# Optimization experiments

Hardware: AMD Instinct MI355X
Metric: run time of the kernel (lower is better)

Reference implementation:

```python
import jax, jax.numpy as jnp
import numpy as np

# ---- module hyperparameters (from init_kwargs) ----
DIM = 16        # Hilbert-space dimension (density matrix is DIM x DIM)
BATCH = 32      # number of initial states evolved in parallel
K_LIND = 4      # number of Lindblad collapse operators
N_TS = 512      # number of Euler integration steps
N_CTRLS = 4     # number of control channels
N_PARAMS = 16   # B-spline control points per channel
DEGREE = 3      # cubic B-splines
T_TOTAL = 1.0
DT = T_TOTAL / N_TS


def _bspline_basis_matrix(t, knots, degree):
    """Cox-de Boor recursion, vectorized over all basis functions.
    t: (n_ts,), knots: (n_knots,). Returns (n_ts, n_knots-1-degree)."""
    k = knots
    # degree-0: indicator of half-open knot spans -> (n_ts, n_knots-1)
    B = ((k[None, :-1] <= t[:, None]) & (t[:, None] < k[None, 1:])).astype(t.dtype)
    for d in range(1, degree + 1):
        left_den = k[d:-1] - k[:-(d + 1)]
        right_den = k[d + 1:] - k[1:-d]
        left = jnp.where(left_den > 0,
                         (t[:, None] - k[None, :-(d + 1)]) / jnp.where(left_den > 0, left_den, 1.0) * B[:, :-1],
                         0.0)
        right = jnp.where(right_den > 0,
                          (k[None, d + 1:] - t[:, None]) / jnp.where(right_den > 0, right_den, 1.0) * B[:, 1:],
                          0.0)
        B = left + right
    return B  # (n_ts, n_knots - 1 - degree) == (n_ts, N_PARAMS)


def setup_inputs() -> dict:
    key = jax.random.key(0)
    ks = jax.random.split(key, 10)
    f32 = jnp.float32
    params = 0.5 * jax.random.normal(ks[0], (N_PARAMS, N_CTRLS), f32)
    H0_re = jax.random.normal(ks[1], (DIM, DIM), f32)
    H0_im = jax.random.normal(ks[2], (DIM, DIM), f32)
    Hc_re = jax.random.normal(ks[3], (N_CTRLS, DIM, DIM), f32)
    Hc_im = jax.random.normal(ks[4], (N_CTRLS, DIM, DIM), f32)
    L_re = 0.3 * jax.random.normal(ks[5], (K_LIND, DIM, DIM), f32)
    L_im = 0.3 * jax.random.normal(ks[6], (K_LIND, DIM, DIM), f32)
    # valid density matrices: rho0 = A A^dag / tr(A A^dag)
    A = (jax.random.normal(ks[7], (BATCH, DIM, DIM), f32)
         + 1j * jax.random.normal(ks[8], (BATCH, DIM, DIM), f32)).astype(jnp.complex64)
    rho0 = jnp.einsum('bij,bkj->bik', A, A.conj())
    tr = jnp.trace(rho0, axis1=-2, axis2=-1).real[:, None, None]
    rho0 = rho0 / tr.astype(jnp.complex64)
    return {
        'params': params,
        'H0_re': H0_re, 'H0_im': H0_im,
        'Hc_re': Hc_re, 'Hc_im': Hc_im,
        'L_re': L_re, 'L_im': L_im,
        'rho0_re': jnp.real(rho0).astype(f32),
        'rho0_im': jnp.imag(rho0).astype(f32),
    }


def reference(params, H0_re, H0_im, Hc_re, Hc_im, L_re, L_im, rho0_re, rho0_im):
    c64 = jnp.complex64
    # Hermitize Hamiltonians
    H0 = (H0_re + 1j * H0_im).astype(c64)
    H0 = 0.5 * (H0 + H0.conj().T)
    Hc = (Hc_re + 1j * Hc_im).astype(c64)
    Hc = 0.5 * (Hc + jnp.conj(jnp.swapaxes(Hc, -1, -2)))
    L = (L_re + 1j * L_im).astype(c64)              # (K, d, d)
    LdL = jnp.einsum('kji,kjl->il', L.conj(), L)    # sum_k L^dag L  (d, d)
    rho0 = (rho0_re + 1j * rho0_im).astype(c64)     # (B, d, d)

    # B-spline control pulses (clamped knot vector, as in evaluate_bspline_batch)
    t = jnp.arange(N_TS, dtype=jnp.float32) * DT
    knots = jnp.concatenate([
        jnp.zeros(DEGREE, jnp.float32),
        jnp.linspace(0.0, T_TOTAL, N_PARAMS - DEGREE + 1).astype(jnp.float32),
        T_TOTAL * jnp.ones(DEGREE, jnp.float32),
    ])
    basis = _bspline_basis_matrix(t, knots, DEGREE)  # (n_ts, n_params)
    u = basis @ params                               # (n_ts, n_ctrls)

    def step(rho, u_t):
        H = H0 + jnp.einsum('c,cij->ij', u_t.astype(c64), Hc)
        jump = jnp.einsum('kij,bjl,kml->bim', L, rho, L.conj())
        drho = (-1j) * (H @ rho - rho @ H) + jump - 0.5 * (LdL @ rho + rho @ LdL)
        rho_new = rho + DT * drho
        pops = jnp.real(jnp.diagonal(rho_new, axis1=-2, axis2=-1)).astype(jnp.float32)
        return rho_new, pops

    _, pops = jax.lax.scan(step, rho0, u)
    return pops  # (n_ts, batch, dim) real populations
```

## Files before the change

### kernel.cpp

```cpp
#include <hip/hip_runtime.h>
#include <hip/hip_bf16.h>

#define DIM    16
#define BATCH  32
#define KL     4
#define NTS    512
#define NC     4
#define NPAR   16
#define DTF    (1.0f/512.0f)
#define BST    40
#define FST    20
#define TST    36

using short8  = __attribute__((ext_vector_type(8))) short;
using short4v = __attribute__((ext_vector_type(4))) short;
using f32x4   = __attribute__((ext_vector_type(4))) float;

__device__ __forceinline__ float b2f(__hip_bfloat16 x) { return __bfloat162float(x); }

__device__ __forceinline__ float ldval(const void* p, int idx, bool isf32) {
  return isf32 ? ((const float*)p)[idx]
               : __bfloat162float(((const __hip_bfloat16*)p)[idx]);
}
__device__ __forceinline__ unsigned short f2bf(float x) {
  unsigned u = __float_as_uint(x);
  unsigned r = u + 0x7FFFu + ((u >> 16) & 1u);
  return (unsigned short)(r >> 16);
}
__device__ __forceinline__ float bf2f(unsigned short h) {
  return __uint_as_float(((unsigned)h) << 16);
}
__device__ __forceinline__ void split2(float v, unsigned short& h, unsigned short& l) {
  unsigned u = __float_as_uint(v);
  h = (unsigned short)(u >> 16);
  float r = v - __uint_as_float(u & 0xFFFF0000u);
  l = (unsigned short)(__float_as_uint(r) >> 16);
}
__device__ __forceinline__ unsigned splitpack(float v) {
  unsigned short h, l;
  split2(v, h, l);
  return (unsigned)h | ((unsigned)l << 16);
}
__device__ __forceinline__ short8 ldfrag(const unsigned short* p) {
  return *(const short8*)p;
}
__device__ __forceinline__ short8 negbf8(short8 a) {
  union { short8 s; unsigned u[4]; } v; v.s = a;
  #pragma unroll
  for (int q = 0; q < 4; ++q) v.u[q] ^= 0x80008000u;
  return v.s;
}
__device__ __forceinline__ f32x4 mm3(short8 Ah, short8 Al, short8 Bh, short8 Bl, f32x4 acc) {
  acc = __builtin_amdgcn_mfma_f32_16x16x32_bf16(Ah, Bh, acc, 0, 0, 0);
  acc = __builtin_amdgcn_mfma_f32_16x16x32_bf16(Al, Bh, acc, 0, 0, 0);
  acc = __builtin_amdgcn_mfma_f32_16x16x32_bf16(Ah, Bl, acc, 0, 0, 0);
  return acc;
}
__device__ __forceinline__ void packfrag(const float* v, short8& hi, short8& lo) {
  union { short8 s; unsigned short e[8]; } H, L;
  #pragma unroll
  for (int q = 0; q < 8; ++q) split2(v[q], H.e[q], L.e[q]);
  hi = H.s; lo = L.s;
}
__device__ __forceinline__ void ldfrag_paired(const unsigned* p, short8& hi, short8& lo) {
  uint4 wa = *(const uint4*)p;
  uint4 wb = *(const uint4*)(p + 4);
  union { short8 s; unsigned u[4]; } H, L;
  H.u[0] = __builtin_amdgcn_perm(wa.y, wa.x, 0x05040100u);
  H.u[1] = __builtin_amdgcn_perm(wa.w, wa.z, 0x05040100u);
  H.u[2] = __builtin_amdgcn_perm(wb.y, wb.x, 0x05040100u);
  H.u[3] = __builtin_amdgcn_perm(wb.w, wb.z, 0x05040100u);
  L.u[0] = __builtin_amdgcn_perm(wa.y, wa.x, 0x07060302u);
  L.u[1] = __builtin_amdgcn_perm(wa.w, wa.z, 0x07060302u);
  L.u[2] = __builtin_amdgcn_perm(wb.y, wb.x, 0x07060302u);
  L.u[3] = __builtin_amdgcn_perm(wb.w, wb.z, 0x07060302u);
  hi = H.s; lo = L.s;
}

__global__ __launch_bounds__(512, 1)
void lindblad_evolve(const void* __restrict__ g_params,
                     const void* __restrict__ g_H0re, const void* __restrict__ g_H0im,
                     const void* __restrict__ g_Hcre, const void* __restrict__ g_Hcim,
                     const void* __restrict__ g_Lre,  const void* __restrict__ g_Lim,
                     const void* __restrict__ g_r0re, const void* __restrict__ g_r0im,
                     float* __restrict__ g_out)
{
  __shared__ __align__(16) unsigned short sPh[16*BST], sPl[16*BST];
  __shared__ __align__(16) unsigned sTp[KL][16*TST];
  __shared__ __align__(16) unsigned short sLh[KL][16*BST], sLl[KL][16*BST];
  __shared__ __align__(16) float sMr[16*FST], sMi[16*FST];
  __shared__ __align__(16) float sU[NTS][NC];
  __shared__ __align__(16) float sPops[NTS*DIM];
  __shared__ int sFlag;

  const int tid = threadIdx.x;
  const int b   = blockIdx.x;
  const int i   = tid >> 4;
  const int j   = tid & 15;
  const int wv  = tid >> 6;
  const int ln  = tid & 63;
  const int fm  = ln & 15;
  const int fq  = ln >> 4;
  const int row0 = fq * 4;
  const int fOff  = fm*BST + fq*8;
  const int fOffS = fm*BST + ((fq*8 + 16) & 31);

  if (tid == 0) sFlag = 0;
  __syncthreads();
  if (tid < 256) {
    float v = b2f(((const __hip_bfloat16*)g_H0re)[tid]);
    if (!(fabsf(v) <= 1e10f)) atomicOr(&sFlag, 1);
  }
  __syncthreads();
  const bool isf32 = (sFlag != 0);

  {
    float kn[20];
    kn[0] = 0.f; kn[1] = 0.f; kn[2] = 0.f;
    #pragma unroll
    for (int q = 0; q < 14; ++q) kn[3 + q] = (float)q / 13.0f;
    kn[17] = 1.f; kn[18] = 1.f; kn[19] = 1.f;
    const float t = (float)tid * DTF;
    float B[19];
    #pragma unroll
    for (int q = 0; q < 19; ++q) B[q] = (kn[q] <= t && t < kn[q+1]) ? 1.f : 0.f;
    #pragma unroll
    for (int d = 1; d <= 3; ++d) {
      #pragma unroll
      for (int q = 0; q + d < 19; ++q) {
        float ld = kn[q+d]   - kn[q];
        float rd = kn[q+d+1] - kn[q+1];
        float lv = (ld > 0.f) ? (t - kn[q])     / ld * B[q]   : 0.f;
        float rv = (rd > 0.f) ? (kn[q+d+1] - t) / rd * B[q+1] : 0.f;
        B[q] = lv + rv;
      }
    }
    #pragma unroll
    for (int c = 0; c < NC; ++c) {
      float s = 0.f;
      #pragma unroll
      for (int q = 0; q < NPAR; ++q) s += B[q] * ldval(g_params, q*NC + c, isf32);
      sU[tid][c] = s;
    }
  }

  if (tid < 256) {
    float* scr = sPops;
    const int ij = i*16 + j, ji = j*16 + i;
    float h0r = 0.5f * (ldval(g_H0re, ij, isf32) + ldval(g_H0re, ji, isf32));
    float h0i = 0.5f * (ldval(g_H0im, ij, isf32) - ldval(g_H0im, ji, isf32));
    float ldr = 0.f, ldi = 0.f;
    for (int k = 0; k < KL; ++k) {
      #pragma unroll
      for (int m = 0; m < DIM; ++m) {
        float ar = ldval(g_Lre, k*256 + m*16 + i, isf32), ai = ldval(g_Lim, k*256 + m*16 + i, isf32);
        float br = ldval(g_Lre, k*256 + m*16 + j, isf32), bi = ldval(g_Lim, k*256 + m*16 + j, isf32);
        ldr += ar*br + ai*bi;
        ldi += ar*bi - ai*br;
      }
    }
    scr[0*256 + ij] =  h0i - 0.5f*ldr;
    scr[1*256 + ij] = -h0r - 0.5f*ldi;
    #pragma unroll
    for (int c = 0; c < NC; ++c) {
      float hr = 0.5f * (ldval(g_Hcre, c*256 + ij, isf32) + ldval(g_Hcre, c*256 + ji, isf32));
      float hi = 0.5f * (ldval(g_Hcim, c*256 + ij, isf32) - ldval(g_Hcim, c*256 + ji, isf32));
      scr[(2 + 2*c)*256 + ij] =  hi;
      scr[(3 + 2*c)*256 + ij] = -hr;
    }
    #pragma unroll
    for (int k = 0; k < KL; ++k) {
      float lr = ldval(g_Lre, k*256 + ij, isf32);
      float li = ldval(g_Lim, k*256 + ij, isf32);
      unsigned short h;
      h = f2bf(lr); sLh[k][i*BST + j]      = h; sLl[k][i*BST + j]      = f2bf(lr - bf2f(h));
      h = f2bf(li); sLh[k][i*BST + 16 + j] = h; sLl[k][i*BST + 16 + j] = f2bf(li - bf2f(h));
    }
    float r0 = ldval(g_r0re, b*256 + ij, isf32);
    float m0 = ldval(g_r0im, b*256 + ij, isf32);
    unsigned short h, l;
    split2(r0, h, l); sPh[j*BST + i]      = h; sPl[j*BST + i]      = l;
    split2(m0, h, l); sPh[j*BST + 16 + i] = h; sPl[j*BST + 16 + i] = l;
  }

  __syncthreads();

  short8 Ah, Al;
  short8 JBh[KL], JBl[KL];
  float  G0v[8], Gcv[NC][8];
  float  rm[4] = {0.f,0.f,0.f,0.f};

  if (wv < 2) {
    const int comp = (fq < 2) ? 0 : 1;
    const int base = (fq & 1) * 8;
    const float* scr = sPops;
    {
      const float* s0 = &scr[comp*256 + fm*16 + base];
      f32x4 va = *(const f32x4*)s0, vb = *(const f32x4*)(s0 + 4);
      #pragma unroll
      for (int q = 0; q < 4; ++q) { G0v[q] = va[q]; G0v[4+q] = vb[q]; }
    }
    #pragma unroll
    for (int c = 0; c < NC; ++c) {
      const float* s0 = &scr[(2 + 2*c + comp)*256 + fm*16 + base];
      f32x4 va = *(const f32x4*)s0, vb = *(const f32x4*)(s0 + 4);
      #pragma unroll
      for (int q = 0; q < 4; ++q) { Gcv[c][q] = va[q]; Gcv[c][4+q] = vb[q]; }
    }
    f32x4 uv = *(const f32x4*)&sU[0][0];
    float gv[8];
    #pragma unroll
    for (int q = 0; q < 8; ++q)
      gv[q] = G0v[q] + uv[0]*Gcv[0][q] + uv[1]*Gcv[1][q] + uv[2]*Gcv[2][q] + uv[3]*Gcv[3][q];
    packfrag(gv, Ah, Al);
    if (wv == 0) {
      #pragma unroll
      for (int k = 0; k < KL; ++k) { JBh[k] = ldfrag(&sLh[k][fOff]); JBl[k] = ldfrag(&sLl[k][fOff]); }
      #pragma unroll
      for (int q = 0; q < 4; ++q) rm[q] = ldval(g_r0re, b*256 + (row0+q)*16 + fm, isf32);
    } else {
      #pragma unroll
      for (int k = 0; k < KL; ++k) {
        short8 h = ldfrag(&sLh[k][fOffS]);
        short8 l = ldfrag(&sLl[k][fOffS]);
        if (fq < 2) { h = negbf8(h); l = negbf8(l); }
        JBh[k] = h; JBl[k] = l;
      }
      #pragma unroll
      for (int q = 0; q < 4; ++q) rm[q] = ldval(g_r0im, b*256 + (row0+q)*16 + fm, isf32);
    }
  } else {
    const int k = (wv < 6) ? (wv - 2) : (wv - 4);
    Ah = ldfrag(&sLh[k][fOff]);
    Al = ldfrag(&sLl[k][fOff]);
  }

  #pragma unroll 1
  for (int t = 0; t < NTS; ++t) {
    __syncthreads();

    f32x4 d1 = {0.f,0.f,0.f,0.f};
    if (wv < 2) {
      short8 Bh, Bl;
      if (wv == 0) {
        Bh = ldfrag(&sPh[fOff]);  Bl = ldfrag(&sPl[fOff]);
        if (fq >= 2) { Bh = negbf8(Bh); Bl = negbf8(Bl); }
      } else {
        Bh = ldfrag(&sPh[fOffS]); Bl = ldfrag(&sPl[fOffS]);
      }
      d1 = mm3(Ah, Al, Bh, Bl, d1);
      float* Mn = (wv == 0) ? sMr : sMi;
      #pragma unroll
      for (int r = 0; r < 4; ++r) Mn[(row0 + r)*FST + fm] = d1[r];
      const int tn = (t + 1 < NTS) ? (t + 1) : t;
      f32x4 uv = *(const f32x4*)&sU[tn][0];
      float gv[8];
      #pragma unroll
      for (int q = 0; q < 8; ++q)
        gv[q] = G0v[q] + uv[0]*Gcv[0][q] + uv[1]*Gcv[1][q] + uv[2]*Gcv[2][q] + uv[3]*Gcv[3][q];
      packfrag(gv, Ah, Al);
    } else {
      const int k = (wv < 6) ? (wv - 2) : (wv - 4);
      if (wv < 4) {
        short8 Brh = ldfrag(&sPh[fOff]),  Brl = ldfrag(&sPl[fOff]);
        if (fq >= 2) { Brh = negbf8(Brh); Brl = negbf8(Brl); }
        short8 Bih = ldfrag(&sPh[fOffS]), Bil = ldfrag(&sPl[fOffS]);
        f32x4 ar = {0.f,0.f,0.f,0.f}, ai = {0.f,0.f,0.f,0.f};
        ar = mm3(Ah, Al, Brh, Brl, ar);
        ai = mm3(Ah, Al, Bih, Bil, ai);
        #pragma unroll
        for (int r = 0; r < 4; ++r) {
          sTp[k][(row0 + r)*TST + fm]      = splitpack(ar[r]);
          sTp[k][(row0 + r)*TST + 16 + fm] = splitpack(ai[r]);
        }
      } else if (wv < 6) {
        short8 Bh = ldfrag(&sPh[fOff]), Bl = ldfrag(&sPl[fOff]);
        if (fq >= 2) { Bh = negbf8(Bh); Bl = negbf8(Bl); }
        f32x4 a = {0.f,0.f,0.f,0.f};
        a = mm3(Ah, Al, Bh, Bl, a);
        #pragma unroll
        for (int r = 0; r < 4; ++r) sTp[k][(row0 + r)*TST + fm] = splitpack(a[r]);
      } else {
        short8 Bh = ldfrag(&sPh[fOffS]), Bl = ldfrag(&sPl[fOffS]);
        f32x4 a = {0.f,0.f,0.f,0.f};
        a = mm3(Ah, Al, Bh, Bl, a);
        #pragma unroll
        for (int r = 0; r < 4; ++r) sTp[k][(row0 + r)*TST + 16 + fm] = splitpack(a[r]);
      }
    }

    __syncthreads();

    if (wv < 2) {
      short8 T0h, T0l, T1h, T1l, T2h, T2l, T3h, T3l;
      ldfrag_paired(&sTp[0][fm*TST + fq*8], T0h, T0l);
      ldfrag_paired(&sTp[1][fm*TST + fq*8], T1h, T1l);
      ldfrag_paired(&sTp[2][fm*TST + fq*8], T2h, T2l);
      ldfrag_paired(&sTp[3][fm*TST + fq*8], T3h, T3l);
      f32x4 a0 = {0.f,0.f,0.f,0.f}, a1 = {0.f,0.f,0.f,0.f},
            a2 = {0.f,0.f,0.f,0.f}, a3 = {0.f,0.f,0.f,0.f};
      a0 = mm3(T0h, T0l, JBh[0], JBl[0], a0);
      a1 = mm3(T1h, T1l, JBh[1], JBl[1], a1);
      a2 = mm3(T2h, T2l, JBh[2], JBl[2], a2);
      a3 = mm3(T3h, T3l, JBh[3], JBl[3], a3);
      const float* Mn = (wv == 0) ? sMr : sMi;
      f32x4 d2 = *(const f32x4*)&Mn[fm*FST + row0];
      union { short4v s; unsigned short e[4]; } HH, LL;
      if (wv == 0) {
        #pragma unroll
        for (int q = 0; q < 4; ++q) {
          rm[q] += DTF * (d1[q] + d2[q] + ((a0[q] + a1[q]) + (a2[q] + a3[q])));
          split2(rm[q], HH.e[q], LL.e[q]);
        }
        *(short4v*)&sPh[fm*BST + row0] = HH.s;
        *(short4v*)&sPl[fm*BST + row0] = LL.s;
        if ((unsigned)(fm - row0) < 4u) sPops[t*DIM + fm] = rm[fm - row0];
      } else {
        #pragma unroll
        for (int q = 0; q < 4; ++q) {
          rm[q] += DTF * (d1[q] - d2[q] + ((a0[q] + a1[q]) + (a2[q] + a3[q])));
          split2(rm[q], HH.e[q], LL.e[q]);
        }
        *(short4v*)&sPh[fm*BST + 16 + row0] = HH.s;
        *(short4v*)&sPl[fm*BST + 16 + row0] = LL.s;
      }
    }
  }

  __syncthreads();
  #pragma unroll
  for (int s = 0; s < NTS*DIM/512; ++s) {
    int idx = s*512 + tid;
    g_out[(idx >> 4)*(BATCH*DIM) + b*DIM + (idx & 15)] = sPops[idx];
  }
}

extern "C" void kernel_launch(void* const* d_in, const int* in_sizes, int n_in,
                              void* d_out, int out_size, void* d_ws, size_t ws_size,
                              hipStream_t stream) {
  (void)out_size; (void)d_ws; (void)ws_size;
  const void *P, *H0r, *H0i, *Hcr, *Hci, *Lr, *Li, *R0r, *R0i;
  int idx64 = -1;
  for (int q = 0; q < n_in; ++q) if (in_sizes[q] == 64) idx64 = q;
  if (idx64 == 6) {
    H0i = d_in[0]; H0r = d_in[1];
    Hci = d_in[2]; Hcr = d_in[3];
    Li  = d_in[4]; Lr  = d_in[5];
    P   = d_in[6];
    R0i = d_in[7]; R0r = d_in[8];
  } else {
    P   = d_in[0];
    H0r = d_in[1]; H0i = d_in[2];
    Hcr = d_in[3]; Hci = d_in[4];
    Lr  = d_in[5]; Li  = d_in[6];
    R0r = d_in[7]; R0i = d_in[8];
  }
  lindblad_evolve<<<dim3(BATCH), dim3(512), 0, stream>>>(
      P, H0r, H0i, Hcr, Hci, Lr, Li, R0r, R0i, (float*)d_out);
}
```

Baseline: 441.1 us.

## Shrink block to two waves, each computing all L·rho products itself

Cuts the workgroup from eight waves to two. Each wave now runs the Hamiltonian product and all four L·rho MFMA products for its real or imaginary half, instead of spreading those products over six extra waves. The goal is to make the per-step __syncthreads barriers cheaper and drop the idle waves, which matters in this latency-bound 512-step loop. In exchange each wave serialises five MFMA chains per step and holds more fragment registers. The output write is also vectorised to float4 stores.

```diff
diff --git a/kernel.cpp b/kernel.cpp
--- a/kernel.cpp
+++ b/kernel.cpp
@@ -77,7 +77,7 @@
   hi = H.s; lo = L.s;
 }
 
-__global__ __launch_bounds__(512, 1)
+__global__ __launch_bounds__(128, 1)
 void lindblad_evolve(const void* __restrict__ g_params,
                      const void* __restrict__ g_H0re, const void* __restrict__ g_H0im,
                      const void* __restrict__ g_Hcre, const void* __restrict__ g_Hcim,
@@ -95,8 +95,6 @@
 
   const int tid = threadIdx.x;
   const int b   = blockIdx.x;
-  const int i   = tid >> 4;
-  const int j   = tid & 15;
   const int wv  = tid >> 6;
   const int ln  = tid & 63;
   const int fm  = ln & 15;
@@ -107,9 +105,10 @@
 
   if (tid == 0) sFlag = 0;
   __syncthreads();
-  if (tid < 256) {
-    float v = b2f(((const __hip_bfloat16*)g_H0re)[tid]);
-    if (!(fabsf(v) <= 1e10f)) atomicOr(&sFlag, 1);
+  {
+    float v0 = b2f(((const __hip_bfloat16*)g_H0re)[tid]);
+    float v1 = b2f(((const __hip_bfloat16*)g_H0re)[tid + 128]);
+    if (!(fabsf(v0) <= 1e10f) || !(fabsf(v1) <= 1e10f)) atomicOr(&sFlag, 1);
   }
   __syncthreads();
   const bool isf32 = (sFlag != 0);
@@ -120,32 +119,35 @@
     #pragma unroll
     for (int q = 0; q < 14; ++q) kn[3 + q] = (float)q / 13.0f;
     kn[17] = 1.f; kn[18] = 1.f; kn[19] = 1.f;
-    const float t = (float)tid * DTF;
-    float B[19];
-    #pragma unroll
-    for (int q = 0; q < 19; ++q) B[q] = (kn[q] <= t && t < kn[q+1]) ? 1.f : 0.f;
-    #pragma unroll
-    for (int d = 1; d <= 3; ++d) {
-      #pragma unroll
-      for (int q = 0; q + d < 19; ++q) {
-        float ld = kn[q+d]   - kn[q];
-        float rd = kn[q+d+1] - kn[q+1];
-        float lv = (ld > 0.f) ? (t - kn[q])     / ld * B[q]   : 0.f;
-        float rv = (rd > 0.f) ? (kn[q+d+1] - t) / rd * B[q+1] : 0.f;
-        B[q] = lv + rv;
-      }
-    }
-    #pragma unroll
-    for (int c = 0; c < NC; ++c) {
-      float s = 0.f;
-      #pragma unroll
-      for (int q = 0; q < NPAR; ++q) s += B[q] * ldval(g_params, q*NC + c, isf32);
-      sU[tid][c] = s;
-    }
-  }
-
-  if (tid < 256) {
+    for (int ts = tid; ts < NTS; ts += 128) {
+      const float t = (float)ts * DTF;
+      float B[19];
+      #pragma unroll
+      for (int q = 0; q < 19; ++q) B[q] = (kn[q] <= t && t < kn[q+1]) ? 1.f : 0.f;
+      #pragma unroll
+      for (int d = 1; d <= 3; ++d) {
+        #pragma unroll
+        for (int q = 0; q + d < 19; ++q) {
+          float ld = kn[q+d]   - kn[q];
+          float rd = kn[q+d+1] - kn[q+1];
+          float lv = (ld > 0.f) ? (t - kn[q])     / ld * B[q]   : 0.f;
+          float rv = (rd > 0.f) ? (kn[q+d+1] - t) / rd * B[q+1] : 0.f;
+          B[q] = lv + rv;
+        }
+      }
+      #pragma unroll
+      for (int c = 0; c < NC; ++c) {
+        float s = 0.f;
+        #pragma unroll
+        for (int q = 0; q < NPAR; ++q) s += B[q] * ldval(g_params, q*NC + c, isf32);
+        sU[ts][c] = s;
+      }
+    }
+  }
+
+  for (int e = tid; e < 256; e += 128) {
     float* scr = sPops;
+    const int i = e >> 4, j = e & 15;
     const int ij = i*16 + j, ji = j*16 + i;
     float h0r = 0.5f * (ldval(g_H0re, ij, isf32) + ldval(g_H0re, ji, isf32));
     float h0i = 0.5f * (ldval(g_H0im, ij, isf32) - ldval(g_H0im, ji, isf32));
@@ -185,12 +187,12 @@
 
   __syncthreads();
 
-  short8 Ah, Al;
+  float  G0v[8], Gcv[NC][8];
+  short8 Lfh[KL], Lfl[KL];
   short8 JBh[KL], JBl[KL];
-  float  G0v[8], Gcv[NC][8];
-  float  rm[4] = {0.f,0.f,0.f,0.f};
-
-  if (wv < 2) {
+  short8 Gh, Gl;
+  float  rm[4];
+  {
     const int comp = (fq < 2) ? 0 : 1;
     const int base = (fq & 1) * 8;
     const float* scr = sPops;
@@ -212,10 +214,13 @@
     #pragma unroll
     for (int q = 0; q < 8; ++q)
       gv[q] = G0v[q] + uv[0]*Gcv[0][q] + uv[1]*Gcv[1][q] + uv[2]*Gcv[2][q] + uv[3]*Gcv[3][q];
-    packfrag(gv, Ah, Al);
+    packfrag(gv, Gh, Gl);
+
+    #pragma unroll
+    for (int k = 0; k < KL; ++k) { Lfh[k] = ldfrag(&sLh[k][fOff]); Lfl[k] = ldfrag(&sLl[k][fOff]); }
     if (wv == 0) {
       #pragma unroll
-      for (int k = 0; k < KL; ++k) { JBh[k] = ldfrag(&sLh[k][fOff]); JBl[k] = ldfrag(&sLl[k][fOff]); }
+      for (int k = 0; k < KL; ++k) { JBh[k] = Lfh[k]; JBl[k] = Lfl[k]; }
       #pragma unroll
       for (int q = 0; q < 4; ++q) rm[q] = ldval(g_r0re, b*256 + (row0+q)*16 + fm, isf32);
     } else {
@@ -229,109 +234,90 @@
       #pragma unroll
       for (int q = 0; q < 4; ++q) rm[q] = ldval(g_r0im, b*256 + (row0+q)*16 + fm, isf32);
     }
-  } else {
-    const int k = (wv < 6) ? (wv - 2) : (wv - 4);
-    Ah = ldfrag(&sLh[k][fOff]);
-    Al = ldfrag(&sLl[k][fOff]);
-  }
+  }
+
+  float* const Mn = (wv == 0) ? sMr : sMi;
+  const int toff = (wv == 0) ? 0 : 16;
 
   #pragma unroll 1
   for (int t = 0; t < NTS; ++t) {
     __syncthreads();
 
+    short8 Bh, Bl;
+    if (wv == 0) {
+      Bh = ldfrag(&sPh[fOff]);  Bl = ldfrag(&sPl[fOff]);
+      if (fq >= 2) { Bh = negbf8(Bh); Bl = negbf8(Bl); }
+    } else {
+      Bh = ldfrag(&sPh[fOffS]); Bl = ldfrag(&sPl[fOffS]);
+    }
     f32x4 d1 = {0.f,0.f,0.f,0.f};
-    if (wv < 2) {
-      short8 Bh, Bl;
-      if (wv == 0) {
-        Bh = ldfrag(&sPh[fOff]);  Bl = ldfrag(&sPl[fOff]);
-        if (fq >= 2) { Bh = negbf8(Bh); Bl = negbf8(Bl); }
-      } else {
-        Bh = ldfrag(&sPh[fOffS]); Bl = ldfrag(&sPl[fOffS]);
-      }
-      d1 = mm3(Ah, Al, Bh, Bl, d1);
-      float* Mn = (wv == 0) ? sMr : sMi;
-      #pragma unroll
-      for (int r = 0; r < 4; ++r) Mn[(row0 + r)*FST + fm] = d1[r];
+    d1 = mm3(Gh, Gl, Bh, Bl, d1);
+    f32x4 t0 = {0.f,0.f,0.f,0.f}, t1 = {0.f,0.f,0.f,0.f},
+          t2 = {0.f,0.f,0.f,0.f}, t3 = {0.f,0.f,0.f,0.f};
+    t0 = mm3(Lfh[0], Lfl[0], Bh, Bl, t0);
+    t1 = mm3(Lfh[1], Lfl[1], Bh, Bl, t1);
+    t2 = mm3(Lfh[2], Lfl[2], Bh, Bl, t2);
+    t3 = mm3(Lfh[3], Lfl[3], Bh, Bl, t3);
+    #pragma unroll
+    for (int r = 0; r < 4; ++r) Mn[(row0 + r)*FST + fm] = d1[r];
+    #pragma unroll
+    for (int r = 0; r < 4; ++r) {
+      sTp[0][(row0 + r)*TST + toff + fm] = splitpack(t0[r]);
+      sTp[1][(row0 + r)*TST + toff + fm] = splitpack(t1[r]);
+      sTp[2][(row0 + r)*TST + toff + fm] = splitpack(t2[r]);
+      sTp[3][(row0 + r)*TST + toff + fm] = splitpack(t3[r]);
+    }
+    {
       const int tn = (t + 1 < NTS) ? (t + 1) : t;
       f32x4 uv = *(const f32x4*)&sU[tn][0];
       float gv[8];
       #pragma unroll
       for (int q = 0; q < 8; ++q)
         gv[q] = G0v[q] + uv[0]*Gcv[0][q] + uv[1]*Gcv[1][q] + uv[2]*Gcv[2][q] + uv[3]*Gcv[3][q];
-      packfrag(gv, Ah, Al);
+      packfrag(gv, Gh, Gl);
+    }
+
+    __syncthreads();
+
+    short8 T0h, T0l, T1h, T1l, T2h, T2l, T3h, T3l;
+    ldfrag_paired(&sTp[0][fm*TST + fq*8], T0h, T0l);
+    ldfrag_paired(&sTp[1][fm*TST + fq*8], T1h, T1l);
+    ldfrag_paired(&sTp[2][fm*TST + fq*8], T2h, T2l);
+    ldfrag_paired(&sTp[3][fm*TST + fq*8], T3h, T3l);
+    f32x4 a0 = {0.f,0.f,0.f,0.f}, a1 = {0.f,0.f,0.f,0.f},
+          a2 = {0.f,0.f,0.f,0.f}, a3 = {0.f,0.f,0.f,0.f};
+    a0 = mm3(T0h, T0l, JBh[0], JBl[0], a0);
+    a1 = mm3(T1h, T1l, JBh[1], JBl[1], a1);
+    a2 = mm3(T2h, T2l, JBh[2], JBl[2], a2);
+    a3 = mm3(T3h, T3l, JBh[3], JBl[3], a3);
+    f32x4 d2 = *(const f32x4*)&Mn[fm*FST + row0];
+    union { short4v s; unsigned short e[4]; } HH, LL;
+    if (wv == 0) {
+      #pragma unroll
+      for (int q = 0; q < 4; ++q) {
+        rm[q] += DTF * (d1[q] + d2[q] + ((a0[q] + a1[q]) + (a2[q] + a3[q])));
+        split2(rm[q], HH.e[q], LL.e[q]);
+      }
+      *(short4v*)&sPh[fm*BST + row0] = HH.s;
+      *(short4v*)&sPl[fm*BST + row0] = LL.s;
+      if ((unsigned)(fm - row0) < 4u) sPops[t*DIM + fm] = rm[fm - row0];
     } else {
-      const int k = (wv < 6) ? (wv - 2) : (wv - 4);
-      if (wv < 4) {
-        short8 Brh = ldfrag(&sPh[fOff]),  Brl = ldfrag(&sPl[fOff]);
-        if (fq >= 2) { Brh = negbf8(Brh); Brl = negbf8(Brl); }
-        short8 Bih = ldfrag(&sPh[fOffS]), Bil = ldfrag(&sPl[fOffS]);
-        f32x4 ar = {0.f,0.f,0.f,0.f}, ai = {0.f,0.f,0.f,0.f};
-        ar = mm3(Ah, Al, Brh, Brl, ar);
-        ai = mm3(Ah, Al, Bih, Bil, ai);
-        #pragma unroll
-        for (int r = 0; r < 4; ++r) {
-          sTp[k][(row0 + r)*TST + fm]      = splitpack(ar[r]);
-          sTp[k][(row0 + r)*TST + 16 + fm] = splitpack(ai[r]);
-        }
-      } else if (wv < 6) {
-        short8 Bh = ldfrag(&sPh[fOff]), Bl = ldfrag(&sPl[fOff]);
-        if (fq >= 2) { Bh = negbf8(Bh); Bl = negbf8(Bl); }
-        f32x4 a = {0.f,0.f,0.f,0.f};
-        a = mm3(Ah, Al, Bh, Bl, a);
-        #pragma unroll
-        for (int r = 0; r < 4; ++r) sTp[k][(row0 + r)*TST + fm] = splitpack(a[r]);
-      } else {
-        short8 Bh = ldfrag(&sPh[fOffS]), Bl = ldfrag(&sPl[fOffS]);
-        f32x4 a = {0.f,0.f,0.f,0.f};
-        a = mm3(Ah, Al, Bh, Bl, a);
-        #pragma unroll
-        for (int r = 0; r < 4; ++r) sTp[k][(row0 + r)*TST + 16 + fm] = splitpack(a[r]);
-      }
-    }
-
-    __syncthreads();
-
-    if (wv < 2) {
-      short8 T0h, T0l, T1h, T1l, T2h, T2l, T3h, T3l;
-      ldfrag_paired(&sTp[0][fm*TST + fq*8], T0h, T0l);
-      ldfrag_paired(&sTp[1][fm*TST + fq*8], T1h, T1l);
-      ldfrag_paired(&sTp[2][fm*TST + fq*8], T2h, T2l);
-      ldfrag_paired(&sTp[3][fm*TST + fq*8], T3h, T3l);
-      f32x4 a0 = {0.f,0.f,0.f,0.f}, a1 = {0.f,0.f,0.f,0.f},
-            a2 = {0.f,0.f,0.f,0.f}, a3 = {0.f,0.f,0.f,0.f};
-      a0 = mm3(T0h, T0l, JBh[0], JBl[0], a0);
-      a1 = mm3(T1h, T1l, JBh[1], JBl[1], a1);
-      a2 = mm3(T2h, T2l, JBh[2], JBl[2], a2);
-      a3 = mm3(T3h, T3l, JBh[3], JBl[3], a3);
-      const float* Mn = (wv == 0) ? sMr : sMi;
-      f32x4 d2 = *(const f32x4*)&Mn[fm*FST + row0];
-      union { short4v s; unsigned short e[4]; } HH, LL;
-      if (wv == 0) {
-        #pragma unroll
-        for (int q = 0; q < 4; ++q) {
-          rm[q] += DTF * (d1[q] + d2[q] + ((a0[q] + a1[q]) + (a2[q] + a3[q])));
-          split2(rm[q], HH.e[q], LL.e[q]);
-        }
-        *(short4v*)&sPh[fm*BST + row0] = HH.s;
-        *(short4v*)&sPl[fm*BST + row0] = LL.s;
-        if ((unsigned)(fm - row0) < 4u) sPops[t*DIM + fm] = rm[fm - row0];
-      } else {
-        #pragma unroll
-        for (int q = 0; q < 4; ++q) {
-          rm[q] += DTF * (d1[q] - d2[q] + ((a0[q] + a1[q]) + (a2[q] + a3[q])));
-          split2(rm[q], HH.e[q], LL.e[q]);
-        }
-        *(short4v*)&sPh[fm*BST + 16 + row0] = HH.s;
-        *(short4v*)&sPl[fm*BST + 16 + row0] = LL.s;
-      }
+      #pragma unroll
+      for (int q = 0; q < 4; ++q) {
+        rm[q] += DTF * (d1[q] - d2[q] + ((a0[q] + a1[q]) + (a2[q] + a3[q])));
+        split2(rm[q], HH.e[q], LL.e[q]);
+      }
+      *(short4v*)&sPh[fm*BST + 16 + row0] = HH.s;
+      *(short4v*)&sPl[fm*BST + 16 + row0] = LL.s;
     }
   }
 
   __syncthreads();
   #pragma unroll
-  for (int s = 0; s < NTS*DIM/512; ++s) {
-    int idx = s*512 + tid;
-    g_out[(idx >> 4)*(BATCH*DIM) + b*DIM + (idx & 15)] = sPops[idx];
+  for (int s = 0; s < NTS*DIM/(128*4); ++s) {
+    int idx = (s*128 + tid) * 4;
+    int tt = idx >> 4, dd = idx & 15;
+    *(float4*)&g_out[tt*(BATCH*DIM) + b*DIM + dd] = *(const float4*)&sPops[idx];
   }
 }
 
@@ -355,6 +341,6 @@
     Lr  = d_in[5]; Li  = d_in[6];
     R0r = d_in[7]; R0i = d_in[8];
   }
-  lindblad_evolve<<<dim3(BATCH), dim3(512), 0, stream>>>(
+  lindblad_evolve<<<dim3(BATCH), dim3(128), 0, stream>>>(
       P, H0r, H0i, Hcr, Hci, Lr, Li, R0r, R0i, (float*)d_out);
 }
```

Result: slower. 578.0 us (+31.1%).

## Rebalance wave roles across 6 waves and decouple commutator from jump accumulation

Applied to the files above, without the earlier changes.

The block shrinks from 8 to 6 waves. Waves 0-1 now only compute the H·rho product and publish it both normally and transposed. Waves 2-3 each compute the left L·rho products for two collapse operators, and waves 4-5 do the second jump matmul plus the rho update. This removes the idle waves per step and lets the next-step Hamiltonian packing run on waves that no longer sit on the update's critical path. It adds an extra transposed shared buffer and vectorizes the final population store to float4. Fewer waves per barrier may lower sync cost, but each of waves 2-3 now issues twice the MFMA work per step.

```diff
diff --git a/kernel.cpp b/kernel.cpp
--- a/kernel.cpp
+++ b/kernel.cpp
@@ -77,7 +77,7 @@
   hi = H.s; lo = L.s;
 }
 
-__global__ __launch_bounds__(512, 1)
+__global__ __launch_bounds__(384, 1)
 void lindblad_evolve(const void* __restrict__ g_params,
                      const void* __restrict__ g_H0re, const void* __restrict__ g_H0im,
                      const void* __restrict__ g_Hcre, const void* __restrict__ g_Hcim,
@@ -88,15 +88,14 @@
   __shared__ __align__(16) unsigned short sPh[16*BST], sPl[16*BST];
   __shared__ __align__(16) unsigned sTp[KL][16*TST];
   __shared__ __align__(16) unsigned short sLh[KL][16*BST], sLl[KL][16*BST];
-  __shared__ __align__(16) float sMr[16*FST], sMi[16*FST];
+  __shared__ __align__(16) float sMr[16*FST],  sMi[16*FST];
+  __shared__ __align__(16) float sMrT[16*FST], sMiT[16*FST];
   __shared__ __align__(16) float sU[NTS][NC];
   __shared__ __align__(16) float sPops[NTS*DIM];
   __shared__ int sFlag;
 
   const int tid = threadIdx.x;
   const int b   = blockIdx.x;
-  const int i   = tid >> 4;
-  const int j   = tid & 15;
   const int wv  = tid >> 6;
   const int ln  = tid & 63;
   const int fm  = ln & 15;
@@ -120,32 +119,35 @@
     #pragma unroll
     for (int q = 0; q < 14; ++q) kn[3 + q] = (float)q / 13.0f;
     kn[17] = 1.f; kn[18] = 1.f; kn[19] = 1.f;
-    const float t = (float)tid * DTF;
-    float B[19];
-    #pragma unroll
-    for (int q = 0; q < 19; ++q) B[q] = (kn[q] <= t && t < kn[q+1]) ? 1.f : 0.f;
-    #pragma unroll
-    for (int d = 1; d <= 3; ++d) {
-      #pragma unroll
-      for (int q = 0; q + d < 19; ++q) {
-        float ld = kn[q+d]   - kn[q];
-        float rd = kn[q+d+1] - kn[q+1];
-        float lv = (ld > 0.f) ? (t - kn[q])     / ld * B[q]   : 0.f;
-        float rv = (rd > 0.f) ? (kn[q+d+1] - t) / rd * B[q+1] : 0.f;
-        B[q] = lv + rv;
-      }
-    }
-    #pragma unroll
-    for (int c = 0; c < NC; ++c) {
-      float s = 0.f;
-      #pragma unroll
-      for (int q = 0; q < NPAR; ++q) s += B[q] * ldval(g_params, q*NC + c, isf32);
-      sU[tid][c] = s;
+    for (int ts = tid; ts < NTS; ts += 384) {
+      const float t = (float)ts * DTF;
+      float B[19];
+      #pragma unroll
+      for (int q = 0; q < 19; ++q) B[q] = (kn[q] <= t && t < kn[q+1]) ? 1.f : 0.f;
+      #pragma unroll
+      for (int d = 1; d <= 3; ++d) {
+        #pragma unroll
+        for (int q = 0; q + d < 19; ++q) {
+          float ld = kn[q+d]   - kn[q];
+          float rd = kn[q+d+1] - kn[q+1];
+          float lv = (ld > 0.f) ? (t - kn[q])     / ld * B[q]   : 0.f;
+          float rv = (rd > 0.f) ? (kn[q+d+1] - t) / rd * B[q+1] : 0.f;
+          B[q] = lv + rv;
+        }
+      }
+      #pragma unroll
+      for (int c = 0; c < NC; ++c) {
+        float s = 0.f;
+        #pragma unroll
+        for (int q = 0; q < NPAR; ++q) s += B[q] * ldval(g_params, q*NC + c, isf32);
+        sU[ts][c] = s;
+      }
     }
   }
 
   if (tid < 256) {
     float* scr = sPops;
+    const int i = tid >> 4, j = tid & 15;
     const int ij = i*16 + j, ji = j*16 + i;
     float h0r = 0.5f * (ldval(g_H0re, ij, isf32) + ldval(g_H0re, ji, isf32));
     float h0i = 0.5f * (ldval(g_H0im, ij, isf32) - ldval(g_H0im, ji, isf32));
@@ -185,7 +187,7 @@
 
   __syncthreads();
 
-  short8 Ah, Al;
+  short8 Ah, Al, A1h, A1l;
   short8 JBh[KL], JBl[KL];
   float  G0v[8], Gcv[NC][8];
   float  rm[4] = {0.f,0.f,0.f,0.f};
@@ -213,33 +215,31 @@
     for (int q = 0; q < 8; ++q)
       gv[q] = G0v[q] + uv[0]*Gcv[0][q] + uv[1]*Gcv[1][q] + uv[2]*Gcv[2][q] + uv[3]*Gcv[3][q];
     packfrag(gv, Ah, Al);
-    if (wv == 0) {
-      #pragma unroll
-      for (int k = 0; k < KL; ++k) { JBh[k] = ldfrag(&sLh[k][fOff]); JBl[k] = ldfrag(&sLl[k][fOff]); }
-      #pragma unroll
-      for (int q = 0; q < 4; ++q) rm[q] = ldval(g_r0re, b*256 + (row0+q)*16 + fm, isf32);
-    } else {
-      #pragma unroll
-      for (int k = 0; k < KL; ++k) {
-        short8 h = ldfrag(&sLh[k][fOffS]);
-        short8 l = ldfrag(&sLl[k][fOffS]);
-        if (fq < 2) { h = negbf8(h); l = negbf8(l); }
-        JBh[k] = h; JBl[k] = l;
-      }
-      #pragma unroll
-      for (int q = 0; q < 4; ++q) rm[q] = ldval(g_r0im, b*256 + (row0+q)*16 + fm, isf32);
-    }
+  } else if (wv < 4) {
+    const int k0 = (wv - 2) * 2;
+    Ah  = ldfrag(&sLh[k0][fOff]);   Al  = ldfrag(&sLl[k0][fOff]);
+    A1h = ldfrag(&sLh[k0+1][fOff]); A1l = ldfrag(&sLl[k0+1][fOff]);
+  } else if (wv == 4) {
+    #pragma unroll
+    for (int k = 0; k < KL; ++k) { JBh[k] = ldfrag(&sLh[k][fOff]); JBl[k] = ldfrag(&sLl[k][fOff]); }
+    #pragma unroll
+    for (int q = 0; q < 4; ++q) rm[q] = ldval(g_r0re, b*256 + (row0+q)*16 + fm, isf32);
   } else {
-    const int k = (wv < 6) ? (wv - 2) : (wv - 4);
-    Ah = ldfrag(&sLh[k][fOff]);
-    Al = ldfrag(&sLl[k][fOff]);
+    #pragma unroll
+    for (int k = 0; k < KL; ++k) {
+      short8 h = ldfrag(&sLh[k][fOffS]);
+      short8 l = ldfrag(&sLl[k][fOffS]);
+      if (fq < 2) { h = negbf8(h); l = negbf8(l); }
+      JBh[k] = h; JBl[k] = l;
+    }
+    #pragma unroll
+    for (int q = 0; q < 4; ++q) rm[q] = ldval(g_r0im, b*256 + (row0+q)*16 + fm, isf32);
   }
 
   #pragma unroll 1
   for (int t = 0; t < NTS; ++t) {
     __syncthreads();
 
-    f32x4 d1 = {0.f,0.f,0.f,0.f};
     if (wv < 2) {
       short8 Bh, Bl;
       if (wv == 0) {
@@ -248,10 +248,13 @@
       } else {
         Bh = ldfrag(&sPh[fOffS]); Bl = ldfrag(&sPl[fOffS]);
       }
-      d1 = mm3(Ah, Al, Bh, Bl, d1);
-      float* Mn = (wv == 0) ? sMr : sMi;
-      #pragma unroll
-      for (int r = 0; r < 4; ++r) Mn[(row0 + r)*FST + fm] = d1[r];
+      f32x4 a = {0.f,0.f,0.f,0.f};
+      a = mm3(Ah, Al, Bh, Bl, a);
+      float* Mn = (wv == 0) ? sMr  : sMi;
+      float* Mt = (wv == 0) ? sMrT : sMiT;
+      #pragma unroll
+      for (int r = 0; r < 4; ++r) Mn[(row0 + r)*FST + fm] = a[r];
+      *(f32x4*)&Mt[fm*FST + row0] = a;
       const int tn = (t + 1 < NTS) ? (t + 1) : t;
       f32x4 uv = *(const f32x4*)&sU[tn][0];
       float gv[8];
@@ -259,39 +262,29 @@
       for (int q = 0; q < 8; ++q)
         gv[q] = G0v[q] + uv[0]*Gcv[0][q] + uv[1]*Gcv[1][q] + uv[2]*Gcv[2][q] + uv[3]*Gcv[3][q];
       packfrag(gv, Ah, Al);
-    } else {
-      const int k = (wv < 6) ? (wv - 2) : (wv - 4);
-      if (wv < 4) {
-        short8 Brh = ldfrag(&sPh[fOff]),  Brl = ldfrag(&sPl[fOff]);
-        if (fq >= 2) { Brh = negbf8(Brh); Brl = negbf8(Brl); }
-        short8 Bih = ldfrag(&sPh[fOffS]), Bil = ldfrag(&sPl[fOffS]);
-        f32x4 ar = {0.f,0.f,0.f,0.f}, ai = {0.f,0.f,0.f,0.f};
-        ar = mm3(Ah, Al, Brh, Brl, ar);
-        ai = mm3(Ah, Al, Bih, Bil, ai);
-        #pragma unroll
-        for (int r = 0; r < 4; ++r) {
-          sTp[k][(row0 + r)*TST + fm]      = splitpack(ar[r]);
-          sTp[k][(row0 + r)*TST + 16 + fm] = splitpack(ai[r]);
-        }
-      } else if (wv < 6) {
-        short8 Bh = ldfrag(&sPh[fOff]), Bl = ldfrag(&sPl[fOff]);
-        if (fq >= 2) { Bh = negbf8(Bh); Bl = negbf8(Bl); }
-        f32x4 a = {0.f,0.f,0.f,0.f};
-        a = mm3(Ah, Al, Bh, Bl, a);
-        #pragma unroll
-        for (int r = 0; r < 4; ++r) sTp[k][(row0 + r)*TST + fm] = splitpack(a[r]);
-      } else {
-        short8 Bh = ldfrag(&sPh[fOffS]), Bl = ldfrag(&sPl[fOffS]);
-        f32x4 a = {0.f,0.f,0.f,0.f};
-        a = mm3(Ah, Al, Bh, Bl, a);
-        #pragma unroll
-        for (int r = 0; r < 4; ++r) sTp[k][(row0 + r)*TST + 16 + fm] = splitpack(a[r]);
+    } else if (wv < 4) {
+      const int k0 = (wv - 2) * 2;
+      short8 Brh = ldfrag(&sPh[fOff]),  Brl = ldfrag(&sPl[fOff]);
+      if (fq >= 2) { Brh = negbf8(Brh); Brl = negbf8(Brl); }
+      short8 Bih = ldfrag(&sPh[fOffS]), Bil = ldfrag(&sPl[fOffS]);
+      f32x4 t0r = {0.f,0.f,0.f,0.f}, t0i = {0.f,0.f,0.f,0.f},
+            t1r = {0.f,0.f,0.f,0.f}, t1i = {0.f,0.f,0.f,0.f};
+      t0r = mm3(Ah,  Al,  Brh, Brl, t0r);
+      t1r = mm3(A1h, A1l, Brh, Brl, t1r);
+      t0i = mm3(Ah,  Al,  Bih, Bil, t0i);
+      t1i = mm3(A1h, A1l, Bih, Bil, t1i);
+      #pragma unroll
+      for (int r = 0; r < 4; ++r) {
+        sTp[k0  ][(row0 + r)*TST + fm]      = splitpack(t0r[r]);
+        sTp[k0  ][(row0 + r)*TST + 16 + fm] = splitpack(t0i[r]);
+        sTp[k0+1][(row0 + r)*TST + fm]      = splitpack(t1r[r]);
+        sTp[k0+1][(row0 + r)*TST + 16 + fm] = splitpack(t1i[r]);
       }
     }
 
     __syncthreads();
 
-    if (wv < 2) {
+    if (wv >= 4) {
       short8 T0h, T0l, T1h, T1l, T2h, T2l, T3h, T3l;
       ldfrag_paired(&sTp[0][fm*TST + fq*8], T0h, T0l);
       ldfrag_paired(&sTp[1][fm*TST + fq*8], T1h, T1l);
@@ -303,10 +296,12 @@
       a1 = mm3(T1h, T1l, JBh[1], JBl[1], a1);
       a2 = mm3(T2h, T2l, JBh[2], JBl[2], a2);
       a3 = mm3(T3h, T3l, JBh[3], JBl[3], a3);
-      const float* Mn = (wv == 0) ? sMr : sMi;
+      const float* Mt = (wv == 4) ? sMrT : sMiT;
+      const float* Mn = (wv == 4) ? sMr  : sMi;
+      f32x4 d1 = *(const f32x4*)&Mt[fm*FST + row0];
       f32x4 d2 = *(const f32x4*)&Mn[fm*FST + row0];
       union { short4v s; unsigned short e[4]; } HH, LL;
-      if (wv == 0) {
+      if (wv == 4) {
         #pragma unroll
         for (int q = 0; q < 4; ++q) {
           rm[q] += DTF * (d1[q] + d2[q] + ((a0[q] + a1[q]) + (a2[q] + a3[q])));
@@ -328,10 +323,10 @@
   }
 
   __syncthreads();
-  #pragma unroll
-  for (int s = 0; s < NTS*DIM/512; ++s) {
-    int idx = s*512 + tid;
-    g_out[(idx >> 4)*(BATCH*DIM) + b*DIM + (idx & 15)] = sPops[idx];
+  for (int idx4 = tid; idx4 < NTS*DIM/4; idx4 += 384) {
+    int idx = idx4 * 4;
+    int tt = idx >> 4, dd = idx & 15;
+    *(float4*)&g_out[tt*(BATCH*DIM) + b*DIM + dd] = *(const float4*)&sPops[idx];
   }
 }
 
@@ -355,6 +350,6 @@
     Lr  = d_in[5]; Li  = d_in[6];
     R0r = d_in[7]; R0i = d_in[8];
   }
-  lindblad_evolve<<<dim3(BATCH), dim3(512), 0, stream>>>(
+  lindblad_evolve<<<dim3(BATCH), dim3(384), 0, stream>>>(
       P, H0r, H0i, Hcr, Hci, Lr, Li, R0r, R0i, (float*)d_out);
 }
```

Result: slower. 518.3 us (+17.5%).
